# Kernel optimization log

Hardware: AMD Instinct MI355X
Metric: run time of the kernel (lower is better)

The kernel has to match this reference:

```python
import jax, jax.numpy as jnp
import numpy as np

MAX_NODES = 1024
FEAT = 64
HID = 32
B, S = 32, 4096


def setup_inputs() -> dict:
    key = jax.random.key(0)
    ks = jax.random.split(key, 9)
    flow_features = jax.random.normal(ks[0], (B, S, FEAT), dtype=jnp.float32)
    src_ips = jax.random.randint(ks[1], (B, S), 0, MAX_NODES, dtype=jnp.int32)
    dst_ips = jax.random.randint(ks[2], (B, S), 0, MAX_NODES, dtype=jnp.int32)
    flow_volumes = jax.random.uniform(ks[3], (B, S), dtype=jnp.float32)
    # learned parameters
    node_emb = jax.random.normal(ks[4], (MAX_NODES, FEAT), dtype=jnp.float32)
    W1 = jax.random.normal(ks[5], (2 * FEAT, HID), dtype=jnp.float32) * (1.0 / np.sqrt(2 * FEAT))
    b1 = jnp.zeros((HID,), dtype=jnp.float32)
    W2 = jax.random.normal(ks[6], (HID, 1), dtype=jnp.float32) * (1.0 / np.sqrt(HID))
    b2 = jnp.zeros((1,), dtype=jnp.float32)
    return {"flow_features": flow_features, "src_ips": src_ips, "dst_ips": dst_ips,
            "flow_volumes": flow_volumes, "node_emb": node_emb,
            "W1": W1, "b1": b1, "W2": W2, "b2": b2}


def reference(flow_features, src_ips, dst_ips, flow_volumes, node_emb, W1, b1, W2, b2):
    b_, s_, f_ = flow_features.shape
    n_ = node_emb.shape[0]
    bidx = jnp.arange(b_)[:, None]  # (B,1) broadcast over seq

    # ---- scatter-add flow features into destination nodes ----
    node_features = jnp.zeros((b_, n_, f_), dtype=flow_features.dtype)
    node_features = node_features.at[bidx, dst_ips].add(flow_features)
    # F.normalize(p=2, dim=-1): x / max(||x||, eps)
    norm = jnp.linalg.norm(node_features, axis=-1, keepdims=True)
    node_features = node_features / jnp.maximum(norm, 1e-12)

    # ---- gather embeddings, edge MLP, scatter weights into adjacency ----
    src_e = node_emb[src_ips]  # (B,S,F)
    dst_e = node_emb[dst_ips]  # (B,S,F)
    h = jax.nn.relu(jnp.concatenate([src_e, dst_e], axis=-1) @ W1 + b1)  # (B,S,32)
    edge_w = jax.nn.sigmoid((h @ W2 + b2)[..., 0])  # (B,S)
    vol_w = jax.nn.sigmoid(flow_volumes / 1000.0)
    w = edge_w * vol_w  # (B,S)

    adjacency = jnp.zeros((b_, n_, n_), dtype=flow_features.dtype)
    # semantics up to scatter ordering of colliding edges)
    adjacency = adjacency.at[bidx, src_ips, dst_ips].set(w)
    adjacency = adjacency.at[bidx, dst_ips, src_ips].set(w)
    return node_features, adjacency
```

## Files before the change

### kernel.cpp

```cpp
#include <hip/hip_runtime.h>
#include <cstdint>
#include <cstddef>

#define BB 32
#define SS 4096
#define FEAT_ 64
#define HID_ 32
#define NN 1024
#define RPB 8

typedef int v4i __attribute__((ext_vector_type(4)));

__global__ void node_feat_kernel(const float* __restrict__ flow,
                                 const int* __restrict__ dst,
                                 float* __restrict__ nf) {
    int row0 = blockIdx.x << 4;
    int b = row0 >> 10;
    __shared__ int sdst[SS];

    const int4* g = (const int4*)(dst + (size_t)b * SS);
    int4* sd4 = (int4*)sdst;
    for (int i = threadIdx.x; i < SS / 4; i += 256) sd4[i] = g[i];
    __syncthreads();

    int wave = threadIdx.x >> 6;
    int lane = threadIdx.x & 63;
    int r0 = row0 + (wave << 2);
    int node0 = r0 & (NN - 1);
    const float* fb = flow + ((size_t)b * SS << 6);

    float acc[4] = {0.f, 0.f, 0.f, 0.f};
    for (int s0 = 0; s0 < SS; s0 += 64) {
        int d = sdst[s0 + lane];
        #pragma unroll
        for (int j = 0; j < 4; ++j) {
            unsigned long long m = __ballot(d == node0 + j);
            while (m) {
                int bit = __ffsll((long long)m) - 1;
                m &= m - 1;
                acc[j] += fb[((s0 + bit) << 6) + lane];
            }
        }
    }

    #pragma unroll
    for (int j = 0; j < 4; ++j) {
        float ss = acc[j] * acc[j];
        #pragma unroll
        for (int off = 32; off > 0; off >>= 1) ss += __shfl_xor(ss, off, 64);
        float v = acc[j] / fmaxf(sqrtf(ss), 1e-12f);
        __builtin_nontemporal_store(v, &nf[((size_t)(r0 + j) << 6) + lane]);
    }
}

__global__ void mlp_kernel(const int* __restrict__ src,
                           const int* __restrict__ dst,
                           const float* __restrict__ vol,
                           const float* __restrict__ emb,
                           const float* __restrict__ W1,
                           const float* __restrict__ b1,
                           const float* __restrict__ W2,
                           const float* __restrict__ b2,
                           float* __restrict__ wout) {
    int i = blockIdx.x * blockDim.x + threadIdx.x;
    int si = src[i], di = dst[i];

    float acc[HID_];
    #pragma unroll
    for (int j = 0; j < HID_; ++j) acc[j] = b1[j];

    #pragma unroll
    for (int half = 0; half < 2; ++half) {
        const float* e = emb + ((half ? di : si) << 6);
        const float* w = W1 + half * 64 * HID_;
        for (int k = 0; k < 64; k += 4) {
            float4 v = *(const float4*)(e + k);
            #pragma unroll
            for (int j = 0; j < HID_; ++j) {
                float a = acc[j];
                a += v.x * w[(k + 0) * HID_ + j];
                a += v.y * w[(k + 1) * HID_ + j];
                a += v.z * w[(k + 2) * HID_ + j];
                a += v.w * w[(k + 3) * HID_ + j];
                acc[j] = a;
            }
        }
    }

    float dotv = b2[0];
    #pragma unroll
    for (int j = 0; j < HID_; ++j) dotv += fmaxf(acc[j], 0.0f) * W2[j];
    float edge_w = 1.0f / (1.0f + expf(-dotv));
    float vol_w  = 1.0f / (1.0f + expf(-vol[i] / 1000.0f));
    wout[i] = edge_w * vol_w;
}

__global__ void adj_dense_kernel(const int* __restrict__ src,
                                 const int* __restrict__ dst,
                                 const float* __restrict__ wbuf,
                                 float* __restrict__ adj) {
    int b  = blockIdx.x >> 7;
    int r0 = (blockIdx.x & 127) << 3;
    int tid = threadIdx.x;

    __shared__ int D[RPB * NN];

    const int* sb = src + (size_t)b * SS;
    const int* db = dst + (size_t)b * SS;
    int svr[16], dvr[16];
    #pragma unroll
    for (int i = 0; i < 16; ++i) {
        svr[i] = sb[tid + (i << 8)];
        dvr[i] = db[tid + (i << 8)];
    }

    int4* D4 = (int4*)D;
    int4 z; z.x = z.y = z.z = z.w = 0;
    #pragma unroll
    for (int i = 0; i < RPB * NN / 4 / 256; ++i) D4[tid + i * 256] = z;
    __syncthreads();

    #pragma unroll
    for (int i = 0; i < 16; ++i) {
        int s = tid + (i << 8);
        unsigned lr1 = (unsigned)(svr[i] - r0);
        if (lr1 < RPB) atomicMax(&D[(lr1 << 10) + dvr[i]], s + 1);
        unsigned lr2 = (unsigned)(dvr[i] - r0);
        if (lr2 < RPB) atomicMax(&D[(lr2 << 10) + svr[i]], SS + s + 1);
    }
    __syncthreads();

    const float* wb = wbuf + (size_t)b * SS;
    #pragma unroll
    for (int i = 0; i < 16; ++i) {
        int s = tid + (i << 8);
        unsigned lr1 = (unsigned)(svr[i] - r0);
        unsigned lr2 = (unsigned)(dvr[i] - r0);
        if ((lr1 < RPB) | (lr2 < RPB)) {
            int wbits = __float_as_int(wb[s]);
            if (lr1 < RPB && D[(lr1 << 10) + dvr[i]] == s + 1)
                D[(lr1 << 10) + dvr[i]] = wbits;
            if (lr2 < RPB && D[(lr2 << 10) + svr[i]] == SS + s + 1)
                D[(lr2 << 10) + svr[i]] = wbits;
        }
    }
    __syncthreads();

    const v4i* Df = (const v4i*)D;
    v4i* out = (v4i*)(adj + ((size_t)b * NN + r0) * NN);
    #pragma unroll
    for (int i = 0; i < RPB * NN / 4 / 256; ++i)
        __builtin_nontemporal_store(Df[tid + i * 256], &out[tid + i * 256]);
}

extern "C" void kernel_launch(void* const* d_in, const int* in_sizes, int n_in,
                              void* d_out, int out_size, void* d_ws, size_t ws_size,
                              hipStream_t stream) {
    const float* flow = (const float*)d_in[0];
    const int*   src  = (const int*)d_in[1];
    const int*   dst  = (const int*)d_in[2];
    const float* vol  = (const float*)d_in[3];
    const float* emb  = (const float*)d_in[4];
    const float* W1   = (const float*)d_in[5];
    const float* b1   = (const float*)d_in[6];
    const float* W2   = (const float*)d_in[7];
    const float* b2   = (const float*)d_in[8];

    float* nf  = (float*)d_out;
    float* adj = nf + (size_t)BB * NN * FEAT_;
    float* wbuf = (float*)d_ws;

    mlp_kernel<<<(BB * SS) / 256, 256, 0, stream>>>(src, dst, vol, emb,
                                                    W1, b1, W2, b2, wbuf);
    adj_dense_kernel<<<BB * (NN / RPB), 256, 0, stream>>>(src, dst, wbuf, adj);
    node_feat_kernel<<<(BB * NN) / 16, 256, 0, stream>>>(flow, dst, nf);
}
```

Before: 242.0 us.

## Zero adjacency in separate kernel and scatter only touched entries

Adds a dedicated grid-stride kernel that zero-fills the dense adjacency with nontemporal stores. The adjacency kernel then writes only the entries touched by edges, instead of copying its whole shared-memory slab to global memory. This separates the bulk zero fill, which should run at full bandwidth, from the resolution logic. In exchange it adds a kernel launch and uncoalesced scattered writes.

```diff
diff --git a/kernel.cpp b/kernel.cpp
--- a/kernel.cpp
+++ b/kernel.cpp
@@ -9,7 +9,15 @@
 #define NN 1024
 #define RPB 8
 
-typedef int v4i __attribute__((ext_vector_type(4)));
+typedef float v4f __attribute__((ext_vector_type(4)));
+
+__global__ void zero_adj_kernel(v4f* __restrict__ adj4, int n4) {
+    int i = blockIdx.x * blockDim.x + threadIdx.x;
+    int stride = gridDim.x * blockDim.x;
+    v4f z = {0.f, 0.f, 0.f, 0.f};
+    for (; i < n4; i += stride)
+        __builtin_nontemporal_store(z, &adj4[i]);
+}
 
 __global__ void node_feat_kernel(const float* __restrict__ flow,
                                  const int* __restrict__ dst,
@@ -95,10 +103,10 @@
     wout[i] = edge_w * vol_w;
 }
 
-__global__ void adj_dense_kernel(const int* __restrict__ src,
-                                 const int* __restrict__ dst,
-                                 const float* __restrict__ wbuf,
-                                 float* __restrict__ adj) {
+__global__ void adj_sparse_kernel(const int* __restrict__ src,
+                                  const int* __restrict__ dst,
+                                  const float* __restrict__ wbuf,
+                                  int* __restrict__ adj) {
     int b  = blockIdx.x >> 7;
     int r0 = (blockIdx.x & 127) << 3;
     int tid = threadIdx.x;
@@ -146,11 +154,16 @@
     }
     __syncthreads();
 
-    const v4i* Df = (const v4i*)D;
-    v4i* out = (v4i*)(adj + ((size_t)b * NN + r0) * NN);
+    int* ab = adj + (size_t)b * NN * NN;
     #pragma unroll
-    for (int i = 0; i < RPB * NN / 4 / 256; ++i)
-        __builtin_nontemporal_store(Df[tid + i * 256], &out[tid + i * 256]);
+    for (int i = 0; i < 16; ++i) {
+        unsigned lr1 = (unsigned)(svr[i] - r0);
+        if (lr1 < RPB)
+            ab[(size_t)(r0 + lr1) * NN + dvr[i]] = D[(lr1 << 10) + dvr[i]];
+        unsigned lr2 = (unsigned)(dvr[i] - r0);
+        if (lr2 < RPB)
+            ab[(size_t)(r0 + lr2) * NN + svr[i]] = D[(lr2 << 10) + svr[i]];
+    }
 }
 
 extern "C" void kernel_launch(void* const* d_in, const int* in_sizes, int n_in,
@@ -170,8 +183,12 @@
     float* adj = nf + (size_t)BB * NN * FEAT_;
     float* wbuf = (float*)d_ws;
 
+    const int adj_f4 = BB * NN * NN / 4;
+
+    zero_adj_kernel<<<2048, 256, 0, stream>>>((v4f*)adj, adj_f4);
     mlp_kernel<<<(BB * SS) / 256, 256, 0, stream>>>(src, dst, vol, emb,
                                                     W1, b1, W2, b2, wbuf);
-    adj_dense_kernel<<<BB * (NN / RPB), 256, 0, stream>>>(src, dst, wbuf, adj);
+    adj_sparse_kernel<<<BB * (NN / RPB), 256, 0, stream>>>(src, dst, wbuf,
+                                                           (int*)adj);
     node_feat_kernel<<<(BB * NN) / 16, 256, 0, stream>>>(flow, dst, nf);
 }
```

After: 293.1 us. 1.21x slower.
